# Performance work log

Hardware: AMD Instinct MI355X
Metric: run time of the kernel (lower is better)

The kernel has to match this reference:

```python
import jax, jax.numpy as jnp
from jax import lax
import numpy as np

B, L, D = 2, 2048, 768
E = 2
DI = E * D          # d_inner = 1536
S = 16              # d_state
K = 4               # d_conv
R = 48              # dt_rank = ceil(D/16)


def setup_inputs() -> dict:
    key = jax.random.key(0)
    ks = jax.random.split(key, 24)
    sc = 0.02  # weight scale for numerical sanity
    inp = {"x": jax.random.normal(ks[0], (B, L, D), jnp.float32)}
    names = ["in_w", "conv_w", "conv_b", "xproj_w", "dt_w", "dt_b", "A_log", "Dp", "out_w"]
    shapes = [(2 * DI, D), (DI, K), (DI,), (R + 2 * S, DI), (DI, R), (DI,), (DI, S), (DI,), (D, DI)]
    i = 1
    for pre in ("f_", "b_"):
        for n, sh in zip(names, shapes):
            scale = 1.0 if n in ("A_log", "Dp", "conv_b", "dt_b") else sc
            inp[pre + n] = jax.random.normal(ks[i], sh, jnp.float32) * scale
            i += 1
    inp["proj_w"] = jax.random.normal(ks[i], (D, 2 * D), jnp.float32) * sc
    inp["proj_b"] = jnp.zeros((D,), jnp.float32)
    inp["ln_g"] = jnp.ones((D,), jnp.float32)
    inp["ln_b"] = jnp.zeros((D,), jnp.float32)
    return inp


def _mamba(x, in_w, conv_w, conv_b, xproj_w, dt_w, dt_b, A_log, Dp, out_w):
    b, l, d = x.shape
    di, k = conv_w.shape
    r = dt_w.shape[1]
    s_ = A_log.shape[1]
    xz = x @ in_w.T                               # [b,l,2*di]
    xc, z = jnp.split(xz, 2, axis=-1)
    # causal depthwise conv over time
    xct = xc.transpose(0, 2, 1)                   # [b,di,l]
    xct = lax.conv_general_dilated(xct, conv_w[:, None, :], (1,), [(k - 1, 0)],
                                   dimension_numbers=('NCH', 'OIH', 'NCH'),
                                   feature_group_count=di)
    xc = jax.nn.silu(xct + conv_b[None, :, None]).transpose(0, 2, 1)  # [b,l,di]
    dbc = xc @ xproj_w.T                          # [b,l,r+2s]
    dt = jax.nn.softplus(dbc[..., :r] @ dt_w.T + dt_b)  # [b,l,di]
    Bm = dbc[..., r:r + s_]                       # [b,l,s]
    Cm = dbc[..., r + s_:]                        # [b,l,s]
    A = -jnp.exp(A_log)                           # [di,s]

    def step(h, inp):
        x_t, dt_t, B_t, C_t = inp
        dA = jnp.exp(dt_t[..., None] * A)         # [b,di,s]
        h = dA * h + dt_t[..., None] * B_t[:, None, :] * x_t[..., None]
        return h, jnp.einsum('bds,bs->bd', h, C_t)

    h0 = jnp.zeros((b, di, s_), x.dtype)
    _, ys = lax.scan(step, h0, (xc.swapaxes(0, 1), dt.swapaxes(0, 1),
                                Bm.swapaxes(0, 1), Cm.swapaxes(0, 1)))
    y = ys.swapaxes(0, 1) + xc * Dp               # D skip connection
    return (y * jax.nn.silu(z)) @ out_w.T


def reference(x, f_in_w, f_conv_w, f_conv_b, f_xproj_w, f_dt_w, f_dt_b, f_A_log, f_Dp, f_out_w,
              b_in_w, b_conv_w, b_conv_b, b_xproj_w, b_dt_w, b_dt_b, b_A_log, b_Dp, b_out_w,
              proj_w, proj_b, ln_g, ln_b):
    fwd = _mamba(x, f_in_w, f_conv_w, f_conv_b, f_xproj_w, f_dt_w, f_dt_b, f_A_log, f_Dp, f_out_w)
    bwd = _mamba(x[:, ::-1], b_in_w, b_conv_w, b_conv_b, b_xproj_w, b_dt_w, b_dt_b,
                 b_A_log, b_Dp, b_out_w)[:, ::-1]
    merged = jnp.concatenate([fwd, bwd], axis=-1)
    out = merged @ proj_w.T + proj_b
    h = x + out
    mu = jnp.mean(h, axis=-1, keepdims=True)
    var = jnp.var(h, axis=-1, keepdims=True)
    return (h - mu) * lax.rsqrt(var + 1e-5) * ln_g + ln_b
```

## Files before the change

### kernel.cpp

```cpp
#include <hip/hip_runtime.h>
#include <math.h>

#define B_   2
#define L_   2048
#define D_   768
#define DI_  1536
#define S_   16
#define R_   48
#define M_   (B_*L_)
#define NC_  32
#define CL_  64

typedef unsigned short ushortT;
typedef __attribute__((ext_vector_type(4))) float f32x4;
typedef __attribute__((ext_vector_type(8))) short short8;

#if __has_builtin(__builtin_amdgcn_exp2f)
#define EXP2F(x) __builtin_amdgcn_exp2f(x)
#define KSC_ 1.4426950408889634f
#else
#define EXP2F(x) __expf(x)
#define KSC_ 1.0f
#endif

__device__ __forceinline__ float siluf(float x) { return x / (1.f + __expf(-x)); }
__device__ __forceinline__ float softplusf(float v) {
    return (v > 20.f) ? v : __logf(1.f + __expf(v));
}

__device__ __forceinline__ ushortT f2bf(float f) {
    unsigned u = __float_as_uint(f);
    unsigned r = (u + 0x7FFFu + ((u >> 16) & 1u)) >> 16;
    return (ushortT)r;
}
__device__ __forceinline__ float bf2f(ushortT h) {
    return __uint_as_float(((unsigned)h) << 16);
}

__device__ __forceinline__ void stage16(const ushortT* g, ushortT* l) {
    __builtin_amdgcn_global_load_lds(
        (const __attribute__((address_space(1))) unsigned int*)g,
        (__attribute__((address_space(3))) unsigned int*)l, 16, 0, 0);
}

__device__ __forceinline__ void storeC(float* p, float v)   { *p = v; }
__device__ __forceinline__ void storeC(ushortT* p, float v) { *p = f2bf(v); }

struct Seg { const float* src; ushortT* dst; long n; int use; int out; };
struct Segs8 { Seg s[8]; };

__global__ __launch_bounds__(256) void convert_all_k(Segs8 S)
{
    const long stride = (long)gridDim.x * 256;
    for (int si = 0; si < 8; ++si) {
        Seg sg = S.s[si];
        if (sg.out == 1) {
            for (long i = blockIdx.x * 256L + threadIdx.x; i < sg.n; i += stride)
                sg.dst[i] = f2bf(sg.src[i]);
        } else {
            for (long i = blockIdx.x * 256L + threadIdx.x; i < sg.n; i += stride) {
                int c = (int)(i % sg.out);
                long r = i / sg.out;
                sg.dst[i] = (c < sg.use) ? f2bf(sg.src[r * sg.use + c]) : (ushortT)0;
            }
        }
    }
}

__global__ __launch_bounds__(256) void transconv_k(
    const float* __restrict__ of, const float* __restrict__ ob,
    ushortT* __restrict__ tf, ushortT* __restrict__ tb)
{
    const int dir = blockIdx.z;
    const float* in = dir ? ob : of;
    ushortT* outp = dir ? tb : tf;
    __shared__ ushortT tile[64][66];
    const int j0 = blockIdx.x * 64;
    const int i0 = blockIdx.y * 64;
    const int tid = threadIdx.x;
    const int dd = tid & 63, qr = tid >> 6;
    #pragma unroll 4
    for (int it = 0; it < 16; ++it) {
        int r = it * 4 + qr;
        tile[r][dd] = f2bf(in[(size_t)(i0 + r) * DI_ + j0 + dd]);
    }
    __syncthreads();
    #pragma unroll 4
    for (int it = 0; it < 16; ++it) {
        int r = it * 4 + qr;
        outp[(size_t)(j0 + r) * D_ + i0 + dd] = tile[dd][r];
    }
}

struct P8 { const ushortT* A[8]; const ushortT* W[8]; void* C[8]; const float* bias[8]; };

template<typename OutT, int EPI, bool NMASK>
__global__ __launch_bounds__(256) void mfma64(
    P8 P, int lda, int ldw, int ldc, int K, int Nreal)
{
    __shared__ ushortT As[128 * 64];
    __shared__ ushortT Ws[128 * 64];
    const ushortT* A = P.A[blockIdx.z];
    const ushortT* W = P.W[blockIdx.z];
    OutT* C = (OutT*)P.C[blockIdx.z];
    const float* bias = P.bias[blockIdx.z];
    const int tid = threadIdx.x;
    const int lane = tid & 63, wid = tid >> 6;
    const int wr = wid >> 1, wc = wid & 1;
    const int m0 = blockIdx.y * 128, n0 = blockIdx.x * 128;

    f32x4 acc[4][4];
    #pragma unroll
    for (int m = 0; m < 4; ++m)
        #pragma unroll
        for (int n = 0; n < 4; ++n)
            acc[m][n] = (f32x4){0.f, 0.f, 0.f, 0.f};

    const int kq = (lane >> 4) * 8;
    const int lr = lane & 15;
    const int srow = tid >> 3;
    const int scolb = (tid & 7) * 16;

    for (int k0 = 0; k0 < K; k0 += 64) {
        #pragma unroll
        for (int r = 0; r < 4; ++r) {
            int row = r * 32 + srow;
            int gcolb = scolb ^ ((row & 7) << 4);
            int lofs = row * 64 + (scolb >> 1);
            stage16(A + (size_t)(m0 + row) * lda + k0 + (gcolb >> 1), As + lofs);
            stage16(W + (size_t)(n0 + row) * ldw + k0 + (gcolb >> 1), Ws + lofs);
        }
        __syncthreads();

        #pragma unroll
        for (int sub = 0; sub < 2; ++sub) {
            short8 afr[4], bfr[4];
            #pragma unroll
            for (int m = 0; m < 4; ++m) {
                int row = wr * 64 + m * 16 + lr;
                int cs = (sub * 32 + kq) ^ ((row & 7) << 3);
                afr[m] = *(const short8*)(As + row * 64 + cs);
            }
            #pragma unroll
            for (int n = 0; n < 4; ++n) {
                int row = wc * 64 + n * 16 + lr;
                int cs = (sub * 32 + kq) ^ ((row & 7) << 3);
                bfr[n] = *(const short8*)(Ws + row * 64 + cs);
            }
            #pragma unroll
            for (int m = 0; m < 4; ++m)
                #pragma unroll
                for (int n = 0; n < 4; ++n)
                    acc[m][n] = __builtin_amdgcn_mfma_f32_16x16x32_bf16(
                        afr[m], bfr[n], acc[m][n], 0, 0, 0);
        }
        __syncthreads();
    }

    #pragma unroll
    for (int m = 0; m < 4; ++m) {
        #pragma unroll
        for (int n = 0; n < 4; ++n) {
            int colg = n0 + wc * 64 + n * 16 + (lane & 15);
            if (NMASK && colg >= Nreal) continue;
            #pragma unroll
            for (int r = 0; r < 4; ++r) {
                int rowg = m0 + wr * 64 + m * 16 + (lane >> 4) * 4 + r;
                float v = acc[m][n][r];
                if (EPI == 2) v = softplusf(v + bias[rowg]);
                storeC(&C[(size_t)rowg * ldc + colg], v);
            }
        }
    }
}

__global__ __launch_bounds__(256) void pack48red_k(
    const float* __restrict__ part,
    float* __restrict__ dbc_f, float* __restrict__ dbc_b,
    ushortT* __restrict__ dbc48_f, ushortT* __restrict__ dbc48_b)
{
    const long n = (long)M_ * 80;
    for (long i = blockIdx.x * 256L + threadIdx.x; i < 2 * n; i += (long)gridDim.x * 256) {
        int dir = (i >= n);
        long j = dir ? i - n : i;
        int col = (int)(j % 80);
        long m = j / 80;
        size_t base = ((size_t)dir * 4 * M_ + m) * 80 + col;
        float sum = part[base] + part[base + (size_t)M_ * 80]
                  + part[base + (size_t)2 * M_ * 80] + part[base + (size_t)3 * M_ * 80];
        (dir ? dbc_b : dbc_f)[m * 80 + col] = sum;
        if (col < 64)
            (dir ? dbc48_b : dbc48_f)[m * 64 + col] = (col < 48) ? f2bf(sum) : (ushortT)0;
    }
}

__global__ __launch_bounds__(256) void conv_fused_k(
    const ushortT* __restrict__ xc_f, const ushortT* __restrict__ xc_b,
    const float* __restrict__ cwf, const float* __restrict__ cwb,
    const float* __restrict__ cbf, const float* __restrict__ cbb,
    ushortT* __restrict__ xcvcat,
    ushortT* __restrict__ xcvt_f, ushortT* __restrict__ xcvt_b)
{
    const int dir = blockIdx.z;
    const ushortT* xc = dir ? xc_b : xc_f;
    const float* cw = dir ? cwb : cwf;
    const float* cb = dir ? cbb : cbf;
    ushortT* xcvt = dir ? xcvt_b : xcvt_f;
    const int dirOff = dir * DI_;

    const int tid = threadIdx.x;
    const int m0 = blockIdx.x * 64;
    const int d0 = blockIdx.y * 64;
    const int b = m0 / L_;
    const int t0 = m0 % L_;
    const int dd = tid & 63;
    const int qr = tid >> 6;

    __shared__ ushortT xt[68][66];
    __shared__ ushortT ot[64][66];

    const int tbase = t0 + (dir ? 0 : -3);
    #pragma unroll 4
    for (int it = 0; it < 17; ++it) {
        int r = it * 4 + qr;
        if (r < 68) {
            int tr = tbase + r;
            ushortT v = 0;
            if (r < 67 && tr >= 0 && tr < L_)
                v = xc[((size_t)b * L_ + tr) * DI_ + d0 + dd];
            xt[r][dd] = v;
        }
    }
    __syncthreads();

    float cwv[4];
    #pragma unroll
    for (int q = 0; q < 4; ++q)
        cwv[q] = dir ? cw[(d0 + dd) * 4 + 3 - q] : cw[(d0 + dd) * 4 + q];
    const float cbv = cb[d0 + dd];

    #pragma unroll 4
    for (int it = 0; it < 16; ++it) {
        int tt = it * 4 + qr;
        float acc = cbv;
        #pragma unroll
        for (int q = 0; q < 4; ++q)
            acc += cwv[q] * bf2f(xt[tt + q][dd]);
        ushortT r16 = f2bf(siluf(acc));
        xcvcat[(size_t)(m0 + tt) * 3072 + dirOff + d0 + dd] = r16;
        ot[tt][dd] = r16;
    }
    __syncthreads();

    #pragma unroll 4
    for (int it = 0; it < 16; ++it) {
        int rr = it * 4 + qr;
        int cc = dd;
        xcvt[(size_t)(d0 + rr) * M_ + m0 + cc] = ot[cc][rr];
    }
}

template<int DIR>
__device__ __forceinline__ void scan1_body(
    const ushortT* __restrict__ xcv_t, const ushortT* __restrict__ dt_t,
    const float* __restrict__ dbc, const float* __restrict__ Alog,
    float* __restrict__ aprod, float* __restrict__ hloc,
    float (*Bs)[16], int c, int b, int d, int half, int tid)
{
    const int t0 = c * CL_;
    #pragma unroll
    for (int it = 0; it < CL_ / 16; ++it) {
        int row = it * 16 + (tid >> 4);
        int col = tid & 15;
        int tau = t0 + row;
        int pos = DIR ? (L_ - 1 - tau) : tau;
        Bs[row][col] = dbc[((size_t)b * L_ + pos) * 80 + R_ + col];
    }
    __syncthreads();

    float A2[8];
    #pragma unroll
    for (int s = 0; s < 8; ++s)
        A2[s] = -__expf(Alog[d * S_ + half * 8 + s]) * KSC_;

    const size_t sbase = (size_t)d * M_ + b * L_;
    float h[8];
    #pragma unroll
    for (int s = 0; s < 8; ++s) h[s] = 0.f;
    float sdt = 0.f;

    for (int g = 0; g < CL_ / 32; ++g) {
        const int t0g = t0 + 32 * g;
        const int tb = DIR ? (L_ - 32 - t0g) : t0g;
        const ushortT* dp = dt_t + sbase + tb;
        const ushortT* xp = xcv_t + sbase + tb;
        short8 d8[4], x8[4];
        #pragma unroll
        for (int v = 0; v < 4; ++v) {
            d8[v] = *(const short8*)(dp + v * 8);
            x8[v] = *(const short8*)(xp + v * 8);
        }
        #pragma unroll
        for (int jj = 0; jj < 32; ++jj) {
            const int q = DIR ? (31 - jj) : jj;
            float dtv = bf2f((ushortT)d8[q >> 3][q & 7]);
            float xv  = bf2f((ushortT)x8[q >> 3][q & 7]);
            float bx = dtv * xv;
            sdt += dtv;
            const int row = 32 * g + jj;
            const f32x4* B4 = (const f32x4*)&Bs[row][0];
            #pragma unroll
            for (int qq = 0; qq < 2; ++qq) {
                f32x4 Bq = B4[half * 2 + qq];
                #pragma unroll
                for (int e2 = 0; e2 < 4; ++e2) {
                    int s = qq * 4 + e2;
                    float a = EXP2F(dtv * A2[s]);
                    h[s] = a * h[s] + bx * Bq[e2];
                }
            }
        }
    }
    size_t idx = ((((size_t)DIR * B_ + b) * NC_ + c) * DI_ + d) * S_ + half * 8;
    #pragma unroll
    for (int qv = 0; qv < 2; ++qv) {
        f32x4 ap, hl;
        #pragma unroll
        for (int e = 0; e < 4; ++e) {
            ap[e] = EXP2F(A2[qv * 4 + e] * sdt);
            hl[e] = h[qv * 4 + e];
        }
        *(f32x4*)(aprod + idx + qv * 4) = ap;
        *(f32x4*)(hloc  + idx + qv * 4) = hl;
    }
}

__global__ __launch_bounds__(256) void scan1_k(
    const ushortT* __restrict__ xcvt_f, const ushortT* __restrict__ dtt_f,
    const float* __restrict__ dbc_f, const float* __restrict__ Af,
    const ushortT* __restrict__ xcvt_b, const ushortT* __restrict__ dtt_b,
    const float* __restrict__ dbc_b, const float* __restrict__ Ab,
    float* __restrict__ aprod, float* __restrict__ hloc)
{
    __shared__ float Bs[CL_][16];
    const int dir = blockIdx.z / NC_, c = blockIdx.z % NC_;
    const int d = blockIdx.x * 128 + (threadIdx.x >> 1);
    const int half = threadIdx.x & 1;
    const int b = blockIdx.y;
    if (dir == 0)
        scan1_body<0>(xcvt_f, dtt_f, dbc_f, Af, aprod, hloc, Bs, c, b, d, half, threadIdx.x);
    else
        scan1_body<1>(xcvt_b, dtt_b, dbc_b, Ab, aprod, hloc, Bs, c, b, d, half, threadIdx.x);
}

__global__ __launch_bounds__(256) void scan2_k(
    float* __restrict__ aprod, const float* __restrict__ hloc)
{
    int q = blockIdx.x * 256 + threadIdx.x;
    if (q >= 2 * B_ * DI_ * S_) return;
    int s = q & 15;
    int t = q >> 4;
    int d = t % DI_;
    int t2 = t / DI_;
    int b = t2 & 1, dir = t2 >> 1;
    float h = 0.f;
    for (int c = 0; c < NC_; ++c) {
        size_t idx = ((((size_t)dir * B_ + b) * NC_ + c) * DI_ + d) * S_ + s;
        float a = aprod[idx], hl = hloc[idx];
        aprod[idx] = h;
        h = hl + a * h;
    }
}

template<int DIR>
__device__ __forceinline__ void scan3_body(
    const ushortT* __restrict__ xcv_t, const ushortT* __restrict__ dt_t,
    const float* __restrict__ dbc, const float* __restrict__ Alog,
    ushortT* __restrict__ y_t, const float* __restrict__ hin,
    float (*Bs)[16], float (*Cs)[16], int c, int b, int d, int half, int tid)
{
    const int t0 = c * CL_;
    #pragma unroll
    for (int it = 0; it < CL_ / 16; ++it) {
        int row = it * 16 + (tid >> 4);
        int col = tid & 15;
        int tau = t0 + row;
        int pos = DIR ? (L_ - 1 - tau) : tau;
        size_t base = ((size_t)b * L_ + pos) * 80 + R_;
        Bs[row][col] = dbc[base + col];
        Cs[row][col] = dbc[base + 16 + col];
    }
    __syncthreads();

    float A2[8];
    #pragma unroll
    for (int s = 0; s < 8; ++s)
        A2[s] = -__expf(Alog[d * S_ + half * 8 + s]) * KSC_;

    size_t idx = ((((size_t)DIR * B_ + b) * NC_ + c) * DI_ + d) * S_ + half * 8;
    float h[8];
    #pragma unroll
    for (int qv = 0; qv < 2; ++qv) {
        f32x4 hv = *(const f32x4*)(hin + idx + qv * 4);
        h[qv * 4 + 0] = hv[0]; h[qv * 4 + 1] = hv[1];
        h[qv * 4 + 2] = hv[2]; h[qv * 4 + 3] = hv[3];
    }

    const size_t sbase = (size_t)d * M_ + b * L_;
    union { ushortT u[4]; unsigned long long v; } pk;

    for (int g = 0; g < CL_ / 32; ++g) {
        const int t0g = t0 + 32 * g;
        const int tb = DIR ? (L_ - 32 - t0g) : t0g;
        const ushortT* dp = dt_t + sbase + tb;
        const ushortT* xp = xcv_t + sbase + tb;
        short8 d8[4], x8[4];
        #pragma unroll
        for (int v = 0; v < 4; ++v) {
            d8[v] = *(const short8*)(dp + v * 8);
            x8[v] = *(const short8*)(xp + v * 8);
        }
        #pragma unroll
        for (int jj = 0; jj < 32; ++jj) {
            const int q = DIR ? (31 - jj) : jj;
            float dtv = bf2f((ushortT)d8[q >> 3][q & 7]);
            float xv  = bf2f((ushortT)x8[q >> 3][q & 7]);
            float bx = dtv * xv;
            const int row = 32 * g + jj;
            const f32x4* B4 = (const f32x4*)&Bs[row][0];
            const f32x4* C4 = (const f32x4*)&Cs[row][0];
            float y = 0.f;
            #pragma unroll
            for (int qq = 0; qq < 2; ++qq) {
                f32x4 Bq = B4[half * 2 + qq];
                f32x4 Cq = C4[half * 2 + qq];
                #pragma unroll
                for (int e2 = 0; e2 < 4; ++e2) {
                    int s = qq * 4 + e2;
                    float a = EXP2F(dtv * A2[s]);
                    h[s] = a * h[s] + bx * Bq[e2];
                    y += h[s] * Cq[e2];
                }
            }
            y += __shfl_xor(y, 1);
            pk.u[DIR ? (3 - (jj & 3)) : (jj & 3)] = f2bf(y);
            if ((jj & 3) == 3 && half == 0) {
                int tst = DIR ? (L_ - 1 - t0g - jj) : (t0g + jj - 3);
                *(unsigned long long*)(y_t + sbase + tst) = pk.v;
            }
        }
    }
}

__global__ __launch_bounds__(256) void scan3_k(
    const ushortT* __restrict__ xcvt_f, const ushortT* __restrict__ dtt_f,
    const float* __restrict__ dbc_f, const float* __restrict__ Af, ushortT* __restrict__ yt_f,
    const ushortT* __restrict__ xcvt_b, const ushortT* __restrict__ dtt_b,
    const float* __restrict__ dbc_b, const float* __restrict__ Ab, ushortT* __restrict__ yt_b,
    const float* __restrict__ hin)
{
    __shared__ float Bs[CL_][16];
    __shared__ float Cs[CL_][16];
    const int dir = blockIdx.z / NC_, c = blockIdx.z % NC_;
    const int d = blockIdx.x * 128 + (threadIdx.x >> 1);
    const int half = threadIdx.x & 1;
    const int b = blockIdx.y;
    if (dir == 0)
        scan3_body<0>(xcvt_f, dtt_f, dbc_f, Af, yt_f, hin, Bs, Cs, c, b, d, half, threadIdx.x);
    else
        scan3_body<1>(xcvt_b, dtt_b, dbc_b, Ab, yt_b, hin, Bs, Cs, c, b, d, half, threadIdx.x);
}

__global__ __launch_bounds__(256) void gate_k(
    const ushortT* __restrict__ y_t_f, const ushortT* __restrict__ y_t_b,
    ushortT* __restrict__ xcvcat,
    const ushortT* __restrict__ z_f, const ushortT* __restrict__ z_b,
    const float* __restrict__ Dp_f, const float* __restrict__ Dp_b)
{
    const int dir = blockIdx.z;
    const ushortT* y_t = dir ? y_t_b : y_t_f;
    const ushortT* z = dir ? z_b : z_f;
    const float* Dp = dir ? Dp_b : Dp_f;
    const int dirOff = dir * DI_;
    const int tid = threadIdx.x;
    const int m0 = blockIdx.x * 64;
    const int d0 = blockIdx.y * 64;
    const int dd = tid & 63;
    const int qr = tid >> 6;
    __shared__ ushortT ys[64][66];
    #pragma unroll 4
    for (int it = 0; it < 16; ++it) {
        int r = it * 4 + qr;
        ys[r][dd] = y_t[(size_t)(d0 + r) * M_ + m0 + dd];
    }
    __syncthreads();
    const float Dpv = Dp[d0 + dd];
    #pragma unroll 4
    for (int it = 0; it < 16; ++it) {
        int mi = it * 4 + qr;
        size_t zi = (size_t)(m0 + mi) * DI_ + d0 + dd;
        size_t xi = (size_t)(m0 + mi) * 3072 + dirOff + d0 + dd;
        float yv = bf2f(ys[dd][mi]);
        float xv = bf2f(xcvcat[xi]);
        float zv = bf2f(z[zi]);
        xcvcat[xi] = f2bf((yv + xv * Dpv) * siluf(zv));
    }
}

__global__ __launch_bounds__(256) void final_ln_k(
    const float* __restrict__ x, const float* __restrict__ acc0,
    const float* __restrict__ acc1, const float* __restrict__ acc2,
    const float* __restrict__ acc3,
    const float* __restrict__ proj_b, const float* __restrict__ ln_g,
    const float* __restrict__ ln_b, float* __restrict__ out)
{
    const int row = blockIdx.x;
    const size_t base = (size_t)row * D_;
    __shared__ float hbuf[D_];
    __shared__ float wsum[4], wsum2[4];
    float s1 = 0.f, s2 = 0.f;
    for (int n = threadIdx.x; n < D_; n += 256) {
        float h = x[base + n] + acc0[base + n] + acc1[base + n]
                + acc2[base + n] + acc3[base + n] + proj_b[n];
        hbuf[n] = h;
        s1 += h; s2 += h * h;
    }
    #pragma unroll
    for (int off = 32; off; off >>= 1) {
        s1 += __shfl_down(s1, off);
        s2 += __shfl_down(s2, off);
    }
    const int wid = threadIdx.x >> 6;
    if ((threadIdx.x & 63) == 0) { wsum[wid] = s1; wsum2[wid] = s2; }
    __syncthreads();
    if (threadIdx.x == 0) {
        float t1 = wsum[0] + wsum[1] + wsum[2] + wsum[3];
        float t2 = wsum2[0] + wsum2[1] + wsum2[2] + wsum2[3];
        float mu = t1 / D_;
        wsum[0] = mu;
        wsum2[0] = t2 / D_ - mu * mu;
    }
    __syncthreads();
    const float mu = wsum[0];
    const float inv = rsqrtf(wsum2[0] + 1e-5f);
    for (int n = threadIdx.x; n < D_; n += 256) {
        out[base + n] = (hbuf[n] - mu) * inv * ln_g[n] + ln_b[n];
    }
}

extern "C" void kernel_launch(void* const* d_in, const int* in_sizes, int n_in,
                              void* d_out, int out_size, void* d_ws, size_t ws_size,
                              hipStream_t stream)
{
    const float* x        = (const float*)d_in[0];
    const float* f_in_w   = (const float*)d_in[1];
    const float* f_conv_w = (const float*)d_in[2];
    const float* f_conv_b = (const float*)d_in[3];
    const float* f_xproj  = (const float*)d_in[4];
    const float* f_dt_w   = (const float*)d_in[5];
    const float* f_dt_bv  = (const float*)d_in[6];
    const float* f_A_log  = (const float*)d_in[7];
    const float* f_Dp     = (const float*)d_in[8];
    const float* f_out_w  = (const float*)d_in[9];
    const float* b_in_w   = (const float*)d_in[10];
    const float* b_conv_w = (const float*)d_in[11];
    const float* b_conv_b = (const float*)d_in[12];
    const float* b_xproj  = (const float*)d_in[13];
    const float* b_dt_w   = (const float*)d_in[14];
    const float* b_dt_bv  = (const float*)d_in[15];
    const float* b_A_log  = (const float*)d_in[16];
    const float* b_Dp     = (const float*)d_in[17];
    const float* b_out_w  = (const float*)d_in[18];
    const float* proj_w   = (const float*)d_in[19];
    const float* proj_b   = (const float*)d_in[20];
    const float* ln_g     = (const float*)d_in[21];
    const float* ln_b     = (const float*)d_in[22];
    float* out = (float*)d_out;

    const size_t TOKH = (size_t)M_ * DI_ / 2;
    float* p = (float*)d_ws;
    ushortT* xbf       = (ushortT*)p;  p += (size_t)M_ * D_ / 2;
    ushortT* projwbf   = (ushortT*)p;  p += (size_t)D_ * DI_ / 2;
    ushortT* inwbf_f   = (ushortT*)p;  p += (size_t)2 * DI_ * D_ / 2;
    ushortT* inwbf_b   = (ushortT*)p;  p += (size_t)2 * DI_ * D_ / 2;
    ushortT* xprojbf_f = (ushortT*)p;  p += (size_t)128 * DI_ / 2;
    ushortT* xprojbf_b = (ushortT*)p;  p += (size_t)128 * DI_ / 2;
    ushortT* dtw_f     = (ushortT*)p;  p += (size_t)DI_ * 64 / 2;
    ushortT* dtw_b     = (ushortT*)p;  p += (size_t)DI_ * 64 / 2;
    ushortT* xc_f      = (ushortT*)p;  p += TOKH;
    ushortT* z_f       = (ushortT*)p;  p += TOKH;
    ushortT* xc_b      = (ushortT*)p;  p += TOKH;
    ushortT* z_b       = (ushortT*)p;  p += TOKH;
    ushortT* xcvcat    = (ushortT*)p;  p += (size_t)M_ * 3072 / 2;
    ushortT* xcvt_f    = (ushortT*)p;  p += TOKH;
    ushortT* xcvt_b    = (ushortT*)p;  p += TOKH;
    ushortT* dtt_f     = (ushortT*)p;  p += TOKH;
    ushortT* dtt_b     = (ushortT*)p;  p += TOKH;
    float*   dbc_f     = p;            p += (size_t)M_ * 80;
    float*   dbc_b     = p;            p += (size_t)M_ * 80;
    ushortT* dbc48_f   = (ushortT*)p;  p += (size_t)M_ * 64 / 2;
    ushortT* dbc48_b   = (ushortT*)p;  p += (size_t)M_ * 64 / 2;
    float*   aprod     = p;            p += (size_t)2 * B_ * NC_ * DI_ * S_;
    float*   hloc      = p;            p += (size_t)2 * B_ * NC_ * DI_ * S_;
    ushortT* Wccat   = inwbf_f;
    ushortT* outwT_f = inwbf_b;
    ushortT* outwT_b = inwbf_b + (size_t)DI_ * D_;
    float*   dbc_part = aprod;
    ushortT* yt_f   = xc_f;
    ushortT* yt_b   = xc_b;
    float*   accb0  = aprod;
    float*   accb1  = hloc;
    float*   accb2  = (float*)xcvt_f;
    float*   accb3  = (float*)xcvt_b;

    dim3 blk(256);

    Segs8 segs;
    segs.s[0] = { x,        xbf,       (long)M_ * D_,      1, 1 };
    segs.s[1] = { proj_w,   projwbf,   (long)D_ * DI_,     1, 1 };
    segs.s[2] = { f_xproj,  xprojbf_f, (long)80 * DI_,     1, 1 };
    segs.s[3] = { b_xproj,  xprojbf_b, (long)80 * DI_,     1, 1 };
    segs.s[4] = { f_dt_w,   dtw_f,     (long)DI_ * 64,    48, 64 };
    segs.s[5] = { b_dt_w,   dtw_b,     (long)DI_ * 64,    48, 64 };
    segs.s[6] = { f_in_w,   inwbf_f,   (long)2 * DI_ * D_, 1, 1 };
    segs.s[7] = { b_in_w,   inwbf_b,   (long)2 * DI_ * D_, 1, 1 };
    convert_all_k<<<1024, blk, 0, stream>>>(segs);

    P8 px = {};
    px.A[0] = px.A[1] = px.A[2] = px.A[3] = xbf;
    px.W[0] = inwbf_f; px.W[1] = inwbf_f + (size_t)DI_ * D_;
    px.W[2] = inwbf_b; px.W[3] = inwbf_b + (size_t)DI_ * D_;
    px.C[0] = xc_f; px.C[1] = z_f; px.C[2] = xc_b; px.C[3] = z_b;
    mfma64<ushortT, 0, false><<<dim3(12, 32, 4), blk, 0, stream>>>(
        px, D_, D_, DI_, D_, 0);

    transconv_k<<<dim3(24, 12, 2), blk, 0, stream>>>(f_out_w, b_out_w, outwT_f, outwT_b);

    P8 pc = {};
    pc.A[0] = projwbf;       pc.A[1] = projwbf + D_;
    pc.W[0] = outwT_f;       pc.W[1] = outwT_b;
    pc.C[0] = Wccat;         pc.C[1] = Wccat + DI_;
    mfma64<ushortT, 0, false><<<dim3(12, 6, 2), blk, 0, stream>>>(
        pc, 2 * D_, D_, 3072, D_, 0);

    conv_fused_k<<<dim3(M_ / 64, DI_ / 64, 2), blk, 0, stream>>>(
        xc_f, xc_b, f_conv_w, b_conv_w, f_conv_b, b_conv_b,
        xcvcat, xcvt_f, xcvt_b);

    P8 pd = {};
    for (int z = 0; z < 8; ++z) {
        int dir = z >> 2, ks = z & 3;
        pd.A[z] = xcvcat + dir * DI_ + ks * 384;
        pd.W[z] = (dir ? xprojbf_b : xprojbf_f) + ks * 384;
        pd.C[z] = dbc_part + (size_t)z * M_ * 80;
    }
    mfma64<float, 0, true><<<dim3(1, 32, 8), blk, 0, stream>>>(
        pd, 3072, DI_, 80, 384, 80);

    pack48red_k<<<1024, blk, 0, stream>>>(dbc_part, dbc_f, dbc_b, dbc48_f, dbc48_b);

    P8 pt = {};
    pt.A[0] = dtw_f;   pt.A[1] = dtw_b;
    pt.W[0] = dbc48_f; pt.W[1] = dbc48_b;
    pt.C[0] = dtt_f;   pt.C[1] = dtt_b;
    pt.bias[0] = f_dt_bv; pt.bias[1] = b_dt_bv;
    mfma64<ushortT, 2, false><<<dim3(32, 12, 2), blk, 0, stream>>>(
        pt, 64, 64, M_, 64, 0);

    scan1_k<<<dim3(DI_ / 128, B_, 2 * NC_), blk, 0, stream>>>(
        xcvt_f, dtt_f, dbc_f, f_A_log, xcvt_b, dtt_b, dbc_b, b_A_log, aprod, hloc);
    scan2_k<<<(2 * B_ * DI_ * S_ + 255) / 256, blk, 0, stream>>>(aprod, hloc);
    scan3_k<<<dim3(DI_ / 128, B_, 2 * NC_), blk, 0, stream>>>(
        xcvt_f, dtt_f, dbc_f, f_A_log, yt_f,
        xcvt_b, dtt_b, dbc_b, b_A_log, yt_b, aprod);

    gate_k<<<dim3(M_ / 64, DI_ / 64, 2), blk, 0, stream>>>(
        yt_f, yt_b, xcvcat, z_f, z_b, f_Dp, b_Dp);

    P8 pf = {};
    pf.A[0] = xcvcat;              pf.W[0] = Wccat;              pf.C[0] = accb0;
    pf.A[1] = xcvcat + 768;        pf.W[1] = Wccat + 768;        pf.C[1] = accb1;
    pf.A[2] = xcvcat + 2 * 768;    pf.W[2] = Wccat + 2 * 768;    pf.C[2] = accb2;
    pf.A[3] = xcvcat + 3 * 768;    pf.W[3] = Wccat + 3 * 768;    pf.C[3] = accb3;
    mfma64<float, 0, false><<<dim3(6, 32, 4), blk, 0, stream>>>(
        pf, 3072, 3072, D_, 768, 0);

    final_ln_k<<<M_, blk, 0, stream>>>(x, accb0, accb1, accb2, accb3,
                                       proj_b, ln_g, ln_b, out);
}
```

Baseline: 295.9 us.

## Fuse gating into scan epilogue and swizzle GEMM workgroup mapping across XCDs

The scan3 kernel now applies the D skip connection and the silu(z) gate itself and writes the gated result directly into the concatenated activation buffer, which removes the separate gate kernel and its transposed y buffer round trip. The GEMM kernel remaps block IDs so that consecutive tiles land on the same XCD for better L2 reuse. The fused stores and z loads are per-timestep scalar accesses with a large stride inside the sequential scan loop, which may add memory latency to the scan.

```diff
diff --git a/kernel.cpp b/kernel.cpp
--- a/kernel.cpp
+++ b/kernel.cpp
@@ -107,7 +107,12 @@
     const int tid = threadIdx.x;
     const int lane = tid & 63, wid = tid >> 6;
     const int wr = wid >> 1, wc = wid & 1;
-    const int m0 = blockIdx.y * 128, n0 = blockIdx.x * 128;
+
+    const int nwg = gridDim.x * gridDim.y;
+    const int bid = blockIdx.y * gridDim.x + blockIdx.x;
+    const int wgid = (bid & 7) * (nwg >> 3) + (bid >> 3);
+    const int m0 = (wgid / gridDim.x) * 128;
+    const int n0 = (wgid % gridDim.x) * 128;
 
     f32x4 acc[4][4];
     #pragma unroll
@@ -376,7 +381,8 @@
 __device__ __forceinline__ void scan3_body(
     const ushortT* __restrict__ xcv_t, const ushortT* __restrict__ dt_t,
     const float* __restrict__ dbc, const float* __restrict__ Alog,
-    ushortT* __restrict__ y_t, const float* __restrict__ hin,
+    const ushortT* __restrict__ zp, const float* __restrict__ Dp,
+    ushortT* __restrict__ xcv_out, const float* __restrict__ hin,
     float (*Bs)[16], float (*Cs)[16], int c, int b, int d, int half, int tid)
 {
     const int t0 = c * CL_;
@@ -396,6 +402,7 @@
     #pragma unroll
     for (int s = 0; s < 8; ++s)
         A2[s] = -__expf(Alog[d * S_ + half * 8 + s]) * KSC_;
+    const float Dpv = Dp[d];
 
     size_t idx = ((((size_t)DIR * B_ + b) * NC_ + c) * DI_ + d) * S_ + half * 8;
     float h[8];
@@ -407,7 +414,6 @@
     }
 
     const size_t sbase = (size_t)d * M_ + b * L_;
-    union { ushortT u[4]; unsigned long long v; } pk;
 
     for (int g = 0; g < CL_ / 32; ++g) {
         const int t0g = t0 + 32 * g;
@@ -443,10 +449,13 @@
                 }
             }
             y += __shfl_xor(y, 1);
-            pk.u[DIR ? (3 - (jj & 3)) : (jj & 3)] = f2bf(y);
-            if ((jj & 3) == 3 && half == 0) {
-                int tst = DIR ? (L_ - 1 - t0g - jj) : (t0g + jj - 3);
-                *(unsigned long long*)(y_t + sbase + tst) = pk.v;
+            if (half == 0) {
+                int tau = t0g + jj;
+                int posw = DIR ? (L_ - 1 - tau) : tau;
+                size_t rowo = (size_t)b * L_ + posw;
+                float zv = bf2f(zp[rowo * DI_ + d]);
+                xcv_out[rowo * 3072 + DIR * DI_ + d] =
+                    f2bf((y + xv * Dpv) * siluf(zv));
             }
         }
     }
@@ -454,10 +463,12 @@
 
 __global__ __launch_bounds__(256) void scan3_k(
     const ushortT* __restrict__ xcvt_f, const ushortT* __restrict__ dtt_f,
-    const float* __restrict__ dbc_f, const float* __restrict__ Af, ushortT* __restrict__ yt_f,
+    const float* __restrict__ dbc_f, const float* __restrict__ Af,
+    const ushortT* __restrict__ z_f, const float* __restrict__ Dp_f,
     const ushortT* __restrict__ xcvt_b, const ushortT* __restrict__ dtt_b,
-    const float* __restrict__ dbc_b, const float* __restrict__ Ab, ushortT* __restrict__ yt_b,
-    const float* __restrict__ hin)
+    const float* __restrict__ dbc_b, const float* __restrict__ Ab,
+    const ushortT* __restrict__ z_b, const float* __restrict__ Dp_b,
+    ushortT* __restrict__ xcvcat, const float* __restrict__ hin)
 {
     __shared__ float Bs[CL_][16];
     __shared__ float Cs[CL_][16];
@@ -466,45 +477,11 @@
     const int half = threadIdx.x & 1;
     const int b = blockIdx.y;
     if (dir == 0)
-        scan3_body<0>(xcvt_f, dtt_f, dbc_f, Af, yt_f, hin, Bs, Cs, c, b, d, half, threadIdx.x);
+        scan3_body<0>(xcvt_f, dtt_f, dbc_f, Af, z_f, Dp_f, xcvcat, hin,
+                      Bs, Cs, c, b, d, half, threadIdx.x);
     else
-        scan3_body<1>(xcvt_b, dtt_b, dbc_b, Ab, yt_b, hin, Bs, Cs, c, b, d, half, threadIdx.x);
-}
-
-__global__ __launch_bounds__(256) void gate_k(
-    const ushortT* __restrict__ y_t_f, const ushortT* __restrict__ y_t_b,
-    ushortT* __restrict__ xcvcat,
-    const ushortT* __restrict__ z_f, const ushortT* __restrict__ z_b,
-    const float* __restrict__ Dp_f, const float* __restrict__ Dp_b)
-{
-    const int dir = blockIdx.z;
-    const ushortT* y_t = dir ? y_t_b : y_t_f;
-    const ushortT* z = dir ? z_b : z_f;
-    const float* Dp = dir ? Dp_b : Dp_f;
-    const int dirOff = dir * DI_;
-    const int tid = threadIdx.x;
-    const int m0 = blockIdx.x * 64;
-    const int d0 = blockIdx.y * 64;
-    const int dd = tid & 63;
-    const int qr = tid >> 6;
-    __shared__ ushortT ys[64][66];
-    #pragma unroll 4
-    for (int it = 0; it < 16; ++it) {
-        int r = it * 4 + qr;
-        ys[r][dd] = y_t[(size_t)(d0 + r) * M_ + m0 + dd];
-    }
-    __syncthreads();
-    const float Dpv = Dp[d0 + dd];
-    #pragma unroll 4
-    for (int it = 0; it < 16; ++it) {
-        int mi = it * 4 + qr;
-        size_t zi = (size_t)(m0 + mi) * DI_ + d0 + dd;
-        size_t xi = (size_t)(m0 + mi) * 3072 + dirOff + d0 + dd;
-        float yv = bf2f(ys[dd][mi]);
-        float xv = bf2f(xcvcat[xi]);
-        float zv = bf2f(z[zi]);
-        xcvcat[xi] = f2bf((yv + xv * Dpv) * siluf(zv));
-    }
+        scan3_body<1>(xcvt_b, dtt_b, dbc_b, Ab, z_b, Dp_b, xcvcat, hin,
+                      Bs, Cs, c, b, d, half, threadIdx.x);
 }
 
 __global__ __launch_bounds__(256) void final_ln_k(
@@ -606,8 +583,6 @@
     ushortT* outwT_f = inwbf_b;
     ushortT* outwT_b = inwbf_b + (size_t)DI_ * D_;
     float*   dbc_part = aprod;
-    ushortT* yt_f   = xc_f;
-    ushortT* yt_b   = xc_b;
     float*   accb0  = aprod;
     float*   accb1  = hloc;
     float*   accb2  = (float*)xcvt_f;
@@ -671,11 +646,9 @@
         xcvt_f, dtt_f, dbc_f, f_A_log, xcvt_b, dtt_b, dbc_b, b_A_log, aprod, hloc);
     scan2_k<<<(2 * B_ * DI_ * S_ + 255) / 256, blk, 0, stream>>>(aprod, hloc);
     scan3_k<<<dim3(DI_ / 128, B_, 2 * NC_), blk, 0, stream>>>(
-        xcvt_f, dtt_f, dbc_f, f_A_log, yt_f,
-        xcvt_b, dtt_b, dbc_b, b_A_log, yt_b, aprod);
-
-    gate_k<<<dim3(M_ / 64, DI_ / 64, 2), blk, 0, stream>>>(
-        yt_f, yt_b, xcvcat, z_f, z_b, f_Dp, b_Dp);
+        xcvt_f, dtt_f, dbc_f, f_A_log, z_f, f_Dp,
+        xcvt_b, dtt_b, dbc_b, b_A_log, z_b, b_Dp,
+        xcvcat, aprod);
 
     P8 pf = {};
     pf.A[0] = xcvcat;              pf.W[0] = Wccat;              pf.C[0] = accb0;
```

Measured after the change: 302.9 us. 1.02x slower.
